# Kernel tuning notes

Measured on AMD Instinct MI355X. Metric: run time of the kernel, lower is better.

Reference implementation:

```python
import jax, jax.numpy as jnp
import numpy as np

# db4 decomposition low-pass filter, pywt coefficient order
DEC_LO = np.array([-0.010597401784997278, 0.032883011666982945,
                   0.030841381835986965, -0.18703481171888114,
                   -0.02798376941698385, 0.6308807679295904,
                   0.7148465705525415, 0.23037781330885523], dtype=np.float32)
LEVEL = 5
B, C, L = 64, 64, 8192


def _qmf_hi(dec_lo):
    # pywt relation: dec_hi[n] = (-1)^(n+1) * dec_lo[F-1-n]
    F = dec_lo.shape[0]
    signs = jnp.where(jnp.arange(F) % 2 == 0, -1.0, 1.0).astype(dec_lo.dtype)
    return signs * dec_lo[::-1]


def _wavedec(x, dec_lo, dec_hi):
    # pywt.dwt(v, w, 'symmetric') == np.convolve(sym_pad(v, F-1), filt, 'valid')[1::2]
    # implemented as a stride-2 cross-correlation with the reversed filter.
    b, c, n = x.shape
    v = x.reshape(b * c, n)
    F = dec_lo.shape[0]
    # kernel: (out_ch=2 [lo, hi], in_ch=1, width=F); reversed => true convolution
    k = jnp.stack([dec_lo[::-1], dec_hi[::-1]])[:, None, :]
    details = []
    for _ in range(LEVEL):
        ext = jnp.pad(v, ((0, 0), (F - 1, F - 1)), mode='symmetric')[:, 1:]
        y = jax.lax.conv_general_dilated(ext[:, None, :], k,
                                         window_strides=(2,), padding='VALID')
        v = y[:, 0, :]           # approximation -> next level input
        details.append(y[:, 1, :])  # detail for this level (finest first)
    approx = v.reshape(b, c, -1)
    # pywt order: [cA_L, cD_L, ..., cD_1] -> coarsest detail first
    det = [d.reshape(b, c, -1) for d in reversed(details)]
    return (approx, *det)


def setup_inputs() -> dict:
    key = jax.random.key(0)
    x = jax.random.normal(key, (B, C, L), dtype=jnp.float32)
    dec_lo = jnp.asarray(DEC_LO)
    dec_hi = _qmf_hi(dec_lo)
    return {"x": x, "dec_lo": dec_lo, "dec_hi": dec_hi}


def reference(x, dec_lo, dec_hi):
    # Returns (cA_L, cD_L, cD_{L-1}, ..., cD_1), matching the torch module's
    # [approx_tensor, detail_tensors] flattened.
    return _wavedec(x, dec_lo, dec_hi)
```

## Files before the change

### kernel.cpp

```cpp
#include <hip/hip_runtime.h>


static constexpr int ROWS = 4096;
static constexpr int N0 = 8192;
static constexpr int L1n = 4099, L2n = 2053, L3n = 1030, L4n = 518, L5n = 262;
static constexpr size_t OFF_D5 = 1073152u;
static constexpr size_t OFF_D4 = 2146304u;
static constexpr size_t OFF_D3 = 4268032u;
static constexpr size_t OFF_D2 = 8486912u;
static constexpr size_t OFF_D1 = 16896000u;

__device__ __forceinline__ float refl_load(const float* __restrict__ s, int idx, int n) {
    int i = (idx < 0) ? (-1 - idx) : ((idx >= n) ? (2 * n - 1 - idx) : idx);
    return s[i];
}

template <typename SRC>
__device__ __forceinline__ void load_window(const SRC* __restrict__ src,
                                            int j, int jmax, float* __restrict__ w) {
    int jb = j < 1 ? 1 : (j > jmax ? jmax : j);
    const float2* __restrict__ s2 = reinterpret_cast<const float2*>(src) + (4 * jb - 3);
#pragma unroll
    for (int t = 0; t < 8; ++t) {
        const float2 v = s2[t];
        w[2 * t] = v.x; w[2 * t + 1] = v.y;
    }
}

template <bool LAST>
__device__ __forceinline__ void dwt_level(
    const float* __restrict__ src, int n, int m,
    const float* __restrict__ h, const float* __restrict__ g,
    float* __restrict__ adst, float* __restrict__ ddst, int tid)
{
    const int ngroups = (m + 3) >> 2;
    const int jmax = (n - 10) >> 3;

    float wc[16], wn[16];
    int j = tid;
    if (j < ngroups) load_window(src, j, jmax, wc);
    while (j < ngroups) {
        const int jn = j + 256;
        if (jn < ngroups) load_window(src, jn, jmax, wn);

        const int p0 = 4 * j;
        if (j >= 1 && j <= jmax && p0 + 3 < m) {
            float aa[4], dd[4];
#pragma unroll
            for (int r = 0; r < 4; ++r) {
                float a = 0.f, d = 0.f;
#pragma unroll
                for (int q = 0; q < 8; ++q) {
                    const float v = wc[2 * r + 7 - q];
                    a = fmaf(h[q], v, a);
                    d = fmaf(g[q], v, d);
                }
                aa[r] = a; dd[r] = d;
            }
#pragma unroll
            for (int r = 0; r < 4; ++r)
                __builtin_nontemporal_store(dd[r], ddst + p0 + r);
            if (LAST) {
#pragma unroll
                for (int r = 0; r < 4; ++r)
                    __builtin_nontemporal_store(aa[r], adst + p0 + r);
            } else {
#pragma unroll
                for (int r = 0; r < 4; ++r) adst[p0 + r] = aa[r];
            }
        } else {
#pragma unroll 4
            for (int r = 0; r < 4; ++r) {
                const int pos = p0 + r;
                if (pos >= m) break;
                const int s0 = 2 * pos + 1;
                float a = 0.f, d = 0.f;
#pragma unroll
                for (int q = 0; q < 8; ++q) {
                    const float v = refl_load(src, s0 - q, n);
                    a = fmaf(h[q], v, a);
                    d = fmaf(g[q], v, d);
                }
                ddst[pos] = d;
                adst[pos] = a;
            }
        }
        j = jn;
#pragma unroll
        for (int t = 0; t < 16; ++t) wc[t] = wn[t];
    }
}

__global__ __launch_bounds__(256, 6)
void wavedec5_kernel(const float* __restrict__ x,
                     const float* __restrict__ dlo,
                     const float* __restrict__ dhi,
                     float* __restrict__ out)
{
    __shared__ __align__(16) float bufA[4100];
    __shared__ __align__(16) float bufB[2056];

    const int row = blockIdx.x;
    const int tid = threadIdx.x;

    float h[8], g[8];
#pragma unroll
    for (int i = 0; i < 8; ++i) { h[i] = dlo[i]; g[i] = dhi[i]; }

    const float* __restrict__ xr = x + (size_t)row * N0;

    dwt_level<false>(xr, N0, L1n, h, g, bufA,
                     out + OFF_D1 + (size_t)row * L1n, tid);
    __syncthreads();
    dwt_level<false>(bufA, L1n, L2n, h, g, bufB,
                     out + OFF_D2 + (size_t)row * L2n, tid);
    __syncthreads();
    dwt_level<false>(bufB, L2n, L3n, h, g, bufA,
                     out + OFF_D3 + (size_t)row * L3n, tid);
    __syncthreads();
    dwt_level<false>(bufA, L3n, L4n, h, g, bufB,
                     out + OFF_D4 + (size_t)row * L4n, tid);
    __syncthreads();
    dwt_level<true>(bufB, L4n, L5n, h, g,
                    out + (size_t)row * L5n,
                    out + OFF_D5 + (size_t)row * L5n, tid);
}

extern "C" void kernel_launch(void* const* d_in, const int* in_sizes, int n_in,
                              void* d_out, int out_size, void* d_ws, size_t ws_size,
                              hipStream_t stream) {
    const float* x   = (const float*)d_in[0];
    const float* dlo = (const float*)d_in[1];
    const float* dhi = (const float*)d_in[2];
    float* out = (float*)d_out;
    wavedec5_kernel<<<ROWS, 256, 0, stream>>>(x, dlo, dhi, out);
}
```

Before: 62.00 us.

## Issue all window loads up front per level with compile-time sizes

Replaces the software-pipelined while loop (one window prefetched ahead) with fully unrolled per-level iterations. Every thread's input windows are loaded before any compute, separated by a sched_barrier, which puts more global loads in flight at once. Sizes become template constants, the remainder groups go to a separate edge path, and nontemporal stores become plain stores. Holding up to 64 window registers per thread led to lowering the occupancy hint from 6 to 4, trading waves per SIMD for memory-level parallelism.

```diff
diff --git a/kernel.cpp b/kernel.cpp
--- a/kernel.cpp
+++ b/kernel.cpp
@@ -15,10 +15,11 @@
     return s[i];
 }
 
-template <typename SRC>
-__device__ __forceinline__ void load_window(const SRC* __restrict__ src,
-                                            int j, int jmax, float* __restrict__ w) {
-    int jb = j < 1 ? 1 : (j > jmax ? jmax : j);
+template <int N>
+__device__ __forceinline__ void load_window(const float* __restrict__ src,
+                                            int j, float* __restrict__ w) {
+    constexpr int jmax = (N - 10) >> 3;
+    const int jb = j < 1 ? 1 : (j > jmax ? jmax : j);
     const float2* __restrict__ s2 = reinterpret_cast<const float2*>(src) + (4 * jb - 3);
 #pragma unroll
     for (int t = 0; t < 8; ++t) {
@@ -27,71 +28,82 @@
     }
 }
 
-template <bool LAST>
+template <int N, int M>
+__device__ __forceinline__ void edge_group(
+    const float* __restrict__ src,
+    const float* __restrict__ h, const float* __restrict__ g,
+    float* __restrict__ adst, float* __restrict__ ddst, int j)
+{
+#pragma unroll 4
+    for (int r = 0; r < 4; ++r) {
+        const int pos = 4 * j + r;
+        if (pos >= M) break;
+        const int s0 = 2 * pos + 1;
+        float a = 0.f, d = 0.f;
+#pragma unroll
+        for (int q = 0; q < 8; ++q) {
+            const float v = refl_load(src, s0 - q, N);
+            a = fmaf(h[q], v, a);
+            d = fmaf(g[q], v, d);
+        }
+        ddst[pos] = d;
+        adst[pos] = a;
+    }
+}
+
+template <int N, int M, int NITER>
 __device__ __forceinline__ void dwt_level(
-    const float* __restrict__ src, int n, int m,
+    const float* __restrict__ src,
     const float* __restrict__ h, const float* __restrict__ g,
     float* __restrict__ adst, float* __restrict__ ddst, int tid)
 {
-    const int ngroups = (m + 3) >> 2;
-    const int jmax = (n - 10) >> 3;
+    constexpr int ngroups = (M + 3) >> 2;
+    constexpr int jmax = (N - 10) >> 3;
+    constexpr int rem = ngroups - NITER * 256;
+    constexpr bool full = (NITER * 256 <= ngroups);
 
-    float wc[16], wn[16];
-    int j = tid;
-    if (j < ngroups) load_window(src, j, jmax, wc);
-    while (j < ngroups) {
-        const int jn = j + 256;
-        if (jn < ngroups) load_window(src, jn, jmax, wn);
+    float w[NITER][16];
+#pragma unroll
+    for (int t = 0; t < NITER; ++t) {
+        const int j = tid + t * 256;
+        if (full || j < ngroups)
+            load_window<N>(src, j, &w[t][0]);
+    }
+    __builtin_amdgcn_sched_barrier(0);
 
+#pragma unroll
+    for (int t = 0; t < NITER; ++t) {
+        const int j = tid + t * 256;
+        if (!full && j >= ngroups) break;
         const int p0 = 4 * j;
-        if (j >= 1 && j <= jmax && p0 + 3 < m) {
+        if (j >= 1 && j <= jmax && p0 + 3 < M) {
             float aa[4], dd[4];
 #pragma unroll
             for (int r = 0; r < 4; ++r) {
                 float a = 0.f, d = 0.f;
 #pragma unroll
                 for (int q = 0; q < 8; ++q) {
-                    const float v = wc[2 * r + 7 - q];
+                    const float v = w[t][2 * r + 7 - q];
                     a = fmaf(h[q], v, a);
                     d = fmaf(g[q], v, d);
                 }
                 aa[r] = a; dd[r] = d;
             }
 #pragma unroll
-            for (int r = 0; r < 4; ++r)
-                __builtin_nontemporal_store(dd[r], ddst + p0 + r);
-            if (LAST) {
+            for (int r = 0; r < 4; ++r) ddst[p0 + r] = dd[r];
 #pragma unroll
-                for (int r = 0; r < 4; ++r)
-                    __builtin_nontemporal_store(aa[r], adst + p0 + r);
-            } else {
-#pragma unroll
-                for (int r = 0; r < 4; ++r) adst[p0 + r] = aa[r];
-            }
+            for (int r = 0; r < 4; ++r) adst[p0 + r] = aa[r];
         } else {
-#pragma unroll 4
-            for (int r = 0; r < 4; ++r) {
-                const int pos = p0 + r;
-                if (pos >= m) break;
-                const int s0 = 2 * pos + 1;
-                float a = 0.f, d = 0.f;
-#pragma unroll
-                for (int q = 0; q < 8; ++q) {
-                    const float v = refl_load(src, s0 - q, n);
-                    a = fmaf(h[q], v, a);
-                    d = fmaf(g[q], v, d);
-                }
-                ddst[pos] = d;
-                adst[pos] = a;
-            }
+            edge_group<N, M>(src, h, g, adst, ddst, j);
         }
-        j = jn;
-#pragma unroll
-        for (int t = 0; t < 16; ++t) wc[t] = wn[t];
+    }
+    if constexpr (rem > 0) {
+        if (tid < rem)
+            edge_group<N, M>(src, h, g, adst, ddst, NITER * 256 + tid);
     }
 }
 
-__global__ __launch_bounds__(256, 6)
+__global__ __launch_bounds__(256, 4)
 void wavedec5_kernel(const float* __restrict__ x,
                      const float* __restrict__ dlo,
                      const float* __restrict__ dhi,
@@ -109,21 +121,21 @@
 
     const float* __restrict__ xr = x + (size_t)row * N0;
 
-    dwt_level<false>(xr, N0, L1n, h, g, bufA,
-                     out + OFF_D1 + (size_t)row * L1n, tid);
+    dwt_level<N0, L1n, 4>(xr, h, g, bufA,
+                          out + OFF_D1 + (size_t)row * L1n, tid);
     __syncthreads();
-    dwt_level<false>(bufA, L1n, L2n, h, g, bufB,
-                     out + OFF_D2 + (size_t)row * L2n, tid);
+    dwt_level<L1n, L2n, 2>(bufA, h, g, bufB,
+                           out + OFF_D2 + (size_t)row * L2n, tid);
     __syncthreads();
-    dwt_level<false>(bufB, L2n, L3n, h, g, bufA,
-                     out + OFF_D3 + (size_t)row * L3n, tid);
+    dwt_level<L2n, L3n, 1>(bufB, h, g, bufA,
+                           out + OFF_D3 + (size_t)row * L3n, tid);
     __syncthreads();
-    dwt_level<false>(bufA, L3n, L4n, h, g, bufB,
-                     out + OFF_D4 + (size_t)row * L4n, tid);
+    dwt_level<L3n, L4n, 1>(bufA, h, g, bufB,
+                           out + OFF_D4 + (size_t)row * L4n, tid);
     __syncthreads();
-    dwt_level<true>(bufB, L4n, L5n, h, g,
-                    out + (size_t)row * L5n,
-                    out + OFF_D5 + (size_t)row * L5n, tid);
+    dwt_level<L4n, L5n, 1>(bufB, h, g,
+                           out + (size_t)row * L5n,
+                           out + OFF_D5 + (size_t)row * L5n, tid);
 }
 
 extern "C" void kernel_launch(void* const* d_in, const int* in_sizes, int n_in,
```

Measured after the change: 58.40 us. 5.8% less time.

## Issue two window loads per thread up front instead of software-pipelined prefetch

Applied to the files above, without the earlier changes.

Replaces the rolling prefetch loop (load next window while computing current) with a split of the groups into two halves, so each thread loads both of its windows before computing either. This raises memory-level parallelism per thread and drops the register copy of the prefetched window. It also removes the nontemporal store hints and lowers the occupancy hint in launch bounds from 6 to 4 waves, giving more registers per thread at the cost of fewer resident blocks.

```diff
diff --git a/kernel.cpp b/kernel.cpp
--- a/kernel.cpp
+++ b/kernel.cpp
@@ -15,11 +15,9 @@
     return s[i];
 }
 
-template <typename SRC>
-__device__ __forceinline__ void load_window(const SRC* __restrict__ src,
-                                            int j, int jmax, float* __restrict__ w) {
-    int jb = j < 1 ? 1 : (j > jmax ? jmax : j);
-    const float2* __restrict__ s2 = reinterpret_cast<const float2*>(src) + (4 * jb - 3);
+__device__ __forceinline__ void load_win(const float* __restrict__ src, int j,
+                                         float* __restrict__ w) {
+    const float2* __restrict__ s2 = reinterpret_cast<const float2*>(src) + (4 * j - 3);
 #pragma unroll
     for (int t = 0; t < 8; ++t) {
         const float2 v = s2[t];
@@ -27,71 +25,79 @@
     }
 }
 
-template <bool LAST>
+__device__ __forceinline__ void compute_store(
+    const float* __restrict__ w,
+    const float* __restrict__ h, const float* __restrict__ g,
+    float* __restrict__ adst, float* __restrict__ ddst, int p0)
+{
+    float aa[4], dd[4];
+#pragma unroll
+    for (int r = 0; r < 4; ++r) {
+        float a = 0.f, d = 0.f;
+#pragma unroll
+        for (int q = 0; q < 8; ++q) {
+            const float v = w[2 * r + 7 - q];
+            a = fmaf(h[q], v, a);
+            d = fmaf(g[q], v, d);
+        }
+        aa[r] = a; dd[r] = d;
+    }
+#pragma unroll
+    for (int r = 0; r < 4; ++r) ddst[p0 + r] = dd[r];
+#pragma unroll
+    for (int r = 0; r < 4; ++r) adst[p0 + r] = aa[r];
+}
+
+__device__ __forceinline__ void edge_group(
+    const float* __restrict__ src, int n, int m,
+    const float* __restrict__ h, const float* __restrict__ g,
+    float* __restrict__ adst, float* __restrict__ ddst, int j)
+{
+#pragma unroll 4
+    for (int r = 0; r < 4; ++r) {
+        const int pos = 4 * j + r;
+        if (pos >= m) break;
+        const int s0 = 2 * pos + 1;
+        float a = 0.f, d = 0.f;
+#pragma unroll
+        for (int q = 0; q < 8; ++q) {
+            const float v = refl_load(src, s0 - q, n);
+            a = fmaf(h[q], v, a);
+            d = fmaf(g[q], v, d);
+        }
+        ddst[pos] = d;
+        adst[pos] = a;
+    }
+}
+
 __device__ __forceinline__ void dwt_level(
     const float* __restrict__ src, int n, int m,
     const float* __restrict__ h, const float* __restrict__ g,
     float* __restrict__ adst, float* __restrict__ ddst, int tid)
 {
-    const int ngroups = (m + 3) >> 2;
+    const int G = (m + 3) >> 2;
+    const int H = (G + 1) >> 1;
     const int jmax = (n - 10) >> 3;
 
-    float wc[16], wn[16];
-    int j = tid;
-    if (j < ngroups) load_window(src, j, jmax, wc);
-    while (j < ngroups) {
-        const int jn = j + 256;
-        if (jn < ngroups) load_window(src, jn, jmax, wn);
+    for (int j = tid; j < H; j += 256) {
+        const int j2 = j + H;
+        const bool v2 = (j2 < G);
+        const bool i1 = (j >= 1) && (j <= jmax) && (4 * j + 3 < m);
+        const bool i2 = v2 && (j2 <= jmax) && (4 * j2 + 3 < m);
 
-        const int p0 = 4 * j;
-        if (j >= 1 && j <= jmax && p0 + 3 < m) {
-            float aa[4], dd[4];
-#pragma unroll
-            for (int r = 0; r < 4; ++r) {
-                float a = 0.f, d = 0.f;
-#pragma unroll
-                for (int q = 0; q < 8; ++q) {
-                    const float v = wc[2 * r + 7 - q];
-                    a = fmaf(h[q], v, a);
-                    d = fmaf(g[q], v, d);
-                }
-                aa[r] = a; dd[r] = d;
-            }
-#pragma unroll
-            for (int r = 0; r < 4; ++r)
-                __builtin_nontemporal_store(dd[r], ddst + p0 + r);
-            if (LAST) {
-#pragma unroll
-                for (int r = 0; r < 4; ++r)
-                    __builtin_nontemporal_store(aa[r], adst + p0 + r);
-            } else {
-#pragma unroll
-                for (int r = 0; r < 4; ++r) adst[p0 + r] = aa[r];
-            }
-        } else {
-#pragma unroll 4
-            for (int r = 0; r < 4; ++r) {
-                const int pos = p0 + r;
-                if (pos >= m) break;
-                const int s0 = 2 * pos + 1;
-                float a = 0.f, d = 0.f;
-#pragma unroll
-                for (int q = 0; q < 8; ++q) {
-                    const float v = refl_load(src, s0 - q, n);
-                    a = fmaf(h[q], v, a);
-                    d = fmaf(g[q], v, d);
-                }
-                ddst[pos] = d;
-                adst[pos] = a;
-            }
-        }
-        j = jn;
-#pragma unroll
-        for (int t = 0; t < 16; ++t) wc[t] = wn[t];
+        float w1[16], w2[16];
+        if (i1) load_win(src, j,  w1);
+        if (i2) load_win(src, j2, w2);
+
+        if (i1) compute_store(w1, h, g, adst, ddst, 4 * j);
+        else    edge_group(src, n, m, h, g, adst, ddst, j);
+
+        if (i2)      compute_store(w2, h, g, adst, ddst, 4 * j2);
+        else if (v2) edge_group(src, n, m, h, g, adst, ddst, j2);
     }
 }
 
-__global__ __launch_bounds__(256, 6)
+__global__ __launch_bounds__(256, 4)
 void wavedec5_kernel(const float* __restrict__ x,
                      const float* __restrict__ dlo,
                      const float* __restrict__ dhi,
@@ -109,21 +115,21 @@
 
     const float* __restrict__ xr = x + (size_t)row * N0;
 
-    dwt_level<false>(xr, N0, L1n, h, g, bufA,
-                     out + OFF_D1 + (size_t)row * L1n, tid);
+    dwt_level(xr, N0, L1n, h, g, bufA,
+              out + OFF_D1 + (size_t)row * L1n, tid);
     __syncthreads();
-    dwt_level<false>(bufA, L1n, L2n, h, g, bufB,
-                     out + OFF_D2 + (size_t)row * L2n, tid);
+    dwt_level(bufA, L1n, L2n, h, g, bufB,
+              out + OFF_D2 + (size_t)row * L2n, tid);
     __syncthreads();
-    dwt_level<false>(bufB, L2n, L3n, h, g, bufA,
-                     out + OFF_D3 + (size_t)row * L3n, tid);
+    dwt_level(bufB, L2n, L3n, h, g, bufA,
+              out + OFF_D3 + (size_t)row * L3n, tid);
     __syncthreads();
-    dwt_level<false>(bufA, L3n, L4n, h, g, bufB,
-                     out + OFF_D4 + (size_t)row * L4n, tid);
+    dwt_level(bufA, L3n, L4n, h, g, bufB,
+              out + OFF_D4 + (size_t)row * L4n, tid);
     __syncthreads();
-    dwt_level<true>(bufB, L4n, L5n, h, g,
-                    out + (size_t)row * L5n,
-                    out + OFF_D5 + (size_t)row * L5n, tid);
+    dwt_level(bufB, L4n, L5n, h, g,
+              out + (size_t)row * L5n,
+              out + OFF_D5 + (size_t)row * L5n, tid);
 }
 
 extern "C" void kernel_launch(void* const* d_in, const int* in_sizes, int n_in,
```

After: 62.42 us. About the same (+0.7%).
